# Performance work log

Measured on AMD Instinct MI355X. Metric: run time of the kernel, lower is better.

The kernel has to match this reference:

```python
import jax, jax.numpy as jnp
import numpy as np

EMBED_DIM = 768
NUM_HEADS = 12
HEAD_DIM = EMBED_DIM // NUM_HEADS
B, S = 2, 2048


def setup_inputs() -> dict:
    key = jax.random.key(0)
    ks = jax.random.split(key, 6)
    glorot = jnp.sqrt(6.0 / (EMBED_DIM + EMBED_DIM)).astype(jnp.float32)
    x = jax.random.normal(ks[0], (B, S, EMBED_DIM), dtype=jnp.float32)
    mask = jnp.zeros((1, 1, S, S), dtype=jnp.float32)  # additive mask, 0 = no masking
    Wq = jax.random.uniform(ks[1], (EMBED_DIM, EMBED_DIM), jnp.float32, -glorot, glorot)
    Wk = jax.random.uniform(ks[2], (EMBED_DIM, EMBED_DIM), jnp.float32, -glorot, glorot)
    Wv = jax.random.uniform(ks[3], (EMBED_DIM, EMBED_DIM), jnp.float32, -glorot, glorot)
    Wo = jax.random.uniform(ks[4], (EMBED_DIM, EMBED_DIM), jnp.float32, -glorot, glorot)
    bo = jnp.zeros((EMBED_DIM,), dtype=jnp.float32)
    return {"x": x, "mask": mask, "Wq": Wq, "Wk": Wk, "Wv": Wv, "Wo": Wo, "bo": bo}


def reference(x, mask, Wq, Wk, Wv, Wo, bo):
    b, s, _ = x.shape
    # Q/K/V projections (no bias), split into heads: [b, h, s, d]
    def split_heads(t):
        return t.reshape(b, s, NUM_HEADS, HEAD_DIM).transpose(0, 2, 1, 3)
    q = split_heads(x @ Wq)
    k = split_heads(x @ Wk)
    v = split_heads(x @ Wv)
    scale = 1.0 / jnp.sqrt(jnp.float32(HEAD_DIM))
    logits = jnp.einsum('bhqd,bhkd->bhqk', q, k) * scale  # [b, h, s, s]
    logits = logits + mask * (-1e9)
    weights = jax.nn.softmax(logits, axis=-1)
    attn = jnp.einsum('bhqk,bhkd->bhqd', weights, v)
    concat = attn.transpose(0, 2, 1, 3).reshape(b, s, EMBED_DIM)
    return concat @ Wo + bo
```

## Files before the change

kernel.cpp:

```cpp
#include <hip/hip_runtime.h>


typedef __bf16 bf16_t;
typedef bf16_t bf16x8 __attribute__((ext_vector_type(8)));
typedef bf16_t bf16x4 __attribute__((ext_vector_type(4)));
typedef float f32x4 __attribute__((ext_vector_type(4)));
typedef _Float16 f16x4 __attribute__((ext_vector_type(4)));

#define SC2 0.1803368801111137f

__device__ __forceinline__ float bf2f(unsigned short u) {
  union { unsigned int i; float f; } x;
  x.i = ((unsigned int)u) << 16;
  return x.f;
}

__device__ __forceinline__ void glds16(const bf16_t* g, bf16_t* l) {
  __builtin_amdgcn_global_load_lds(
      (const __attribute__((address_space(1))) void*)g,
      (__attribute__((address_space(3))) void*)l, 16, 0, 0);
}

__device__ __forceinline__ int detect_bf16_flag(const unsigned short* x) {
  const int lane = threadIdx.x & 63;
  const uint4* p = (const uint4*)x;
  uint4 a = p[lane * 2];
  uint4 b = p[lane * 2 + 1];
  unsigned int w[8] = {a.x, a.y, a.z, a.w, b.x, b.y, b.z, b.w};
  unsigned int big = 0;
#pragma unroll
  for (int i = 0; i < 8; i++) {
    unsigned int e0 = (w[i] >> 7) & 0xFF, e1 = (w[i] >> 23) & 0xFF;
    big |= (e0 > 0x88u) | (e1 > 0x88u);
  }
  unsigned long long bal = __ballot(big != 0u);
  return bal == 0ULL ? 1 : 0;
}

__global__ void k_prep(const void* __restrict__ x, const void* __restrict__ mask,
                       const void* __restrict__ Wq, const void* __restrict__ Wk,
                       const void* __restrict__ Wv, const void* __restrict__ Wo,
                       bf16_t* __restrict__ xb, bf16_t* __restrict__ wqkvT,
                       bf16_t* __restrict__ woT, int* __restrict__ mflags) {
  __shared__ float ts[32][33];
  __shared__ int snz;
  const int blk = blockIdx.x;
  const int f = detect_bf16_flag((const unsigned short*)x);

  if (blk < 1536) {
    int i = blk * 256 + threadIdx.x;
    if (f) {
      ((uint4*)xb)[i] = ((const uint4*)x)[i];
    } else {
      const float* xf = (const float*)x + (size_t)i * 8;
      bf16x8 v;
#pragma unroll
      for (int j = 0; j < 8; j++) v[j] = (bf16_t)xf[j];
      *(bf16x8*)(xb + (size_t)i * 8) = v;
    }
  } else if (blk < 3840) {
    const int t = blk - 1536;
    const int z = t / 576, r = t % 576, kt = r / 24, nt = r % 24;
    const void* wsrc = (z == 0) ? Wq : (z == 1) ? Wk : (z == 2) ? Wv : Wo;
    bf16_t* dst = (z < 3) ? (wqkvT + (size_t)z * 768 * 768) : woT;
    const int c = threadIdx.x & 31, r0 = threadIdx.x >> 5;
#pragma unroll
    for (int i = 0; i < 4; i++) {
      int kr = kt * 32 + r0 + i * 8;
      float v;
      if (f) v = bf2f(((const unsigned short*)wsrc)[(size_t)kr * 768 + nt * 32 + c]);
      else   v = ((const float*)wsrc)[(size_t)kr * 768 + nt * 32 + c];
      ts[r0 + i * 8][c] = v;
    }
    __syncthreads();
#pragma unroll
    for (int i = 0; i < 4; i++) {
      int nr = nt * 32 + r0 + i * 8;
      dst[(size_t)nr * 768 + kt * 32 + c] = (bf16_t)ts[c][r0 + i * 8];
    }
  } else {
    const int t = blk - 3840;
    const int qt = t >> 4, ktm = t & 15;
    if (threadIdx.x == 0) snz = 0;
    __syncthreads();
    int nz = 0;
    for (int i = 0; i < 64; i++) {
      int lin = i * 256 + threadIdx.x;
      int rr = lin >> 7, cc = lin & 127;
      size_t idx = (size_t)(qt * 128 + rr) * 2048 + ktm * 128 + cc;
      float v = f ? bf2f(((const unsigned short*)mask)[idx]) : ((const float*)mask)[idx];
      nz |= (v != 0.0f);
    }
    if (nz) snz = 1;
    __syncthreads();
    if (threadIdx.x == 0) mflags[qt * 16 + ktm] = snz;
  }
}

__global__ __launch_bounds__(256, 2) void k_gemmQKV(
    const bf16_t* __restrict__ A, const bf16_t* __restrict__ Bm,
    bf16_t* __restrict__ Qd, bf16_t* __restrict__ Kd, _Float16* __restrict__ Vt) {
  __shared__ __align__(16) char smem[17408];
  bf16_t* As = (bf16_t*)smem;
  bf16_t* Bs = (bf16_t*)(smem + 8192);
  _Float16* Tb = (_Float16*)smem;

  const int tid = threadIdx.x;
  const int n0 = blockIdx.x * 128, m0 = blockIdx.y * 128;
  const int r = tid >> 2, c8 = (tid & 3) << 3;
  const bf16_t* Ag = A + (size_t)(m0 + r) * 768 + c8;
  const bf16_t* Bg = Bm + (size_t)(n0 + r) * 768 + c8;
  const int wid = tid >> 6, lane = tid & 63;
  const int wm = (wid >> 1) << 6, wn = (wid & 1) << 6;
  const int lr = lane & 15, lk = (lane >> 4) << 3, g4 = (lane >> 4) << 2;

  f32x4 acc[4][4];
  const f32x4 z = {0.f, 0.f, 0.f, 0.f};
#pragma unroll
  for (int i = 0; i < 4; i++)
#pragma unroll
    for (int j = 0; j < 4; j++) acc[i][j] = z;

  for (int k0 = 0; k0 < 768; k0 += 32) {
    glds16(Ag + k0, As + wid * 512);
    glds16(Ag + (size_t)64 * 768 + k0, As + 2048 + wid * 512);
    glds16(Bg + k0, Bs + wid * 512);
    glds16(Bg + (size_t)64 * 768 + k0, Bs + 2048 + wid * 512);
    __syncthreads();
    bf16x8 af[4], bf_[4];
#pragma unroll
    for (int t = 0; t < 4; t++) af[t]  = *(const bf16x8*)&As[(wm + t * 16 + lr) * 32 + lk];
#pragma unroll
    for (int t = 0; t < 4; t++) bf_[t] = *(const bf16x8*)&Bs[(wn + t * 16 + lr) * 32 + lk];
#pragma unroll
    for (int i = 0; i < 4; i++)
#pragma unroll
      for (int j = 0; j < 4; j++)
        acc[i][j] = __builtin_amdgcn_mfma_f32_16x16x32_bf16(af[i], bf_[j], acc[i][j], 0, 0, 0);
    __syncthreads();
  }

  if (n0 < 1536) {
    bf16_t* dst = (n0 < 768) ? Qd : Kd;
    const int nb = (n0 < 768) ? n0 : n0 - 768;
    const int bb = m0 >> 11;
#pragma unroll
    for (int i = 0; i < 4; i++)
#pragma unroll
      for (int j = 0; j < 4; j++) {
        const int rc = nb + wn + j * 16 + lr;
        const int hh = rc >> 6, dd = rc & 63;
        const size_t base = (((size_t)bb * 12 + hh) * 2048) * 64 + dd;
#pragma unroll
        for (int reg = 0; reg < 4; reg++) {
          const int s = (m0 & 2047) + wm + i * 16 + g4 + reg;
          dst[base + (size_t)s * 64] = (bf16_t)acc[i][j][reg];
        }
      }
  } else {
    const int bb = m0 >> 11;
#pragma unroll
    for (int half = 0; half < 2; half++) {
      if ((wid & 1) == half) {
#pragma unroll
        for (int j = 0; j < 4; j++) {
          const int d_l = j * 16 + lr;
#pragma unroll
          for (int i = 0; i < 4; i++)
#pragma unroll
            for (int reg = 0; reg < 4; reg++)
              Tb[d_l * 136 + wm + i * 16 + g4 + reg] = (_Float16)acc[i][j][reg];
        }
      }
      __syncthreads();
      const int row = tid >> 2, cc = (tid & 3) * 32;
      const int vcol = (n0 - 1536) + half * 64 + row;
      const int hh = vcol >> 6;
      _Float16* dstv = Vt + (((size_t)bb * 12 + hh) * 64 + row) * 2048 + (m0 & 2047) + cc;
#pragma unroll
      for (int u = 0; u < 4; u++)
        *(uint4*)(dstv + u * 8) = *(const uint4*)&Tb[row * 136 + cc + u * 8];
      __syncthreads();
    }
  }
}

__global__ __launch_bounds__(320, 4) void k_flash(
    const bf16_t* __restrict__ Qd, const bf16_t* __restrict__ Kd,
    const _Float16* __restrict__ Vt, const void* __restrict__ mask,
    const int* __restrict__ mflags, const unsigned short* __restrict__ xdet,
    bf16_t* __restrict__ attn) {
  __shared__ __align__(16) char sm[32768];

  const int tid = threadIdx.x, wid = tid >> 6, lane = tid & 63;
  const int lr = lane & 15, quad = lane >> 4, lk = quad << 3, g4 = quad << 2;

  const int lin = blockIdx.x;
  const int gx = lin & 7, ww = lin >> 3;
  const int hb = gx * 3 + (ww >> 5);
  const int h = hb % 12, bb = hb / 12;
  const int qt = ww & 31;

  const size_t bh = (size_t)bb * 12 + h;
  const char* Kh = (const char*)(Kd + bh * 2048 * 64);
  const char* Vh = (const char*)(Vt + bh * 64 * 2048);

  if (wid == 4) {
    const char* kS[8]; const char* vS[8];
#pragma unroll
    for (int u = 0; u < 8; u++) {
      const int R = (u >> 1) * 16 + lr;
      const int c = (u & 1) * 4 + quad;
      kS[u] = Kh + R * 128 + c * 16;
      const int u2 = u * 2 + (lane >> 5);
      const int dtv = u2 & 3, ctv = u2 >> 2, j2 = lane & 31;
      vS[u] = Vh + (size_t)(dtv * 16 + (j2 & 15)) * 4096 + ctv * 32 + (j2 >> 4) * 16;
    }
    uint4 kv[8], vv[8];
#pragma unroll
    for (int u = 0; u < 8; u++) kv[u] = *(const uint4*)(kS[u]);
#pragma unroll
    for (int u = 0; u < 8; u++) vv[u] = *(const uint4*)(vS[u]);
#pragma unroll
    for (int u = 0; u < 8; u++) *(uint4*)(sm + u * 1024 + lane * 16) = kv[u];
#pragma unroll
    for (int u = 0; u < 8; u++) *(uint4*)(sm + 8192 + u * 1024 + lane * 16) = vv[u];
    __syncthreads();
    for (int s = 0; s < 32; s++) {
      if (s < 31) {
        const int t = s + 1;
        char* buf = sm + (t & 1) * 16384;
#pragma unroll
        for (int u = 0; u < 8; u++) kv[u] = *(const uint4*)(kS[u] + (size_t)t * 8192);
#pragma unroll
        for (int u = 0; u < 8; u++) vv[u] = *(const uint4*)(vS[u] + (size_t)t * 128);
#pragma unroll
        for (int u = 0; u < 8; u++) *(uint4*)(buf + u * 1024 + lane * 16) = kv[u];
#pragma unroll
        for (int u = 0; u < 8; u++) *(uint4*)(buf + 8192 + u * 1024 + lane * 16) = vv[u];
      }
      __syncthreads();
    }
    return;
  }

  const bf16_t* Qh = Qd + bh * 2048 * 64;
  const int q0 = qt * 64 + wid * 16;
  const int mbf = detect_bf16_flag(xdet);
  const int* mfrow = mflags + (qt >> 1) * 16;

  const bf16x8 qf0 = *(const bf16x8*)&Qh[(size_t)(q0 + lr) * 64 + lk];
  const bf16x8 qf1 = *(const bf16x8*)&Qh[(size_t)(q0 + lr) * 64 + 32 + lk];

  const f32x4 z = {0.f, 0.f, 0.f, 0.f};
  f32x4 ot[4];
#pragma unroll
  for (int dt = 0; dt < 4; dt++) ot[dt] = z;
  float mrow = -1e30f, lrow = 0.f;

  __syncthreads();

  for (int s = 0; s < 32; s++) {
    const char* Kc = sm + (s & 1) * 16384;
    const char* Vc = Kc + 8192;

    f32x4 sv[4];
#pragma unroll
    for (int ct = 0; ct < 4; ct++) sv[ct] = z;
#pragma unroll
    for (int ct = 0; ct < 4; ct++) {
      bf16x8 kf0 = *(const bf16x8*)(Kc + ct * 2048 + lane * 16);
      bf16x8 kf1 = *(const bf16x8*)(Kc + ct * 2048 + 1024 + lane * 16);
      sv[ct] = __builtin_amdgcn_mfma_f32_16x16x32_bf16(kf0, qf0, sv[ct], 0, 0, 0);
      sv[ct] = __builtin_amdgcn_mfma_f32_16x16x32_bf16(kf1, qf1, sv[ct], 0, 0, 0);
    }

    if (mfrow[s >> 1]) {
#pragma unroll
      for (int ct = 0; ct < 4; ct++)
#pragma unroll
        for (int reg = 0; reg < 4; reg++) {
          size_t mi = (size_t)(q0 + lr) * 2048 + s * 64 + ct * 16 + g4 + reg;
          float mv = mbf ? bf2f(((const unsigned short*)mask)[mi])
                         : ((const float*)mask)[mi];
          sv[ct][reg] -= 8e9f * mv;
        }
    }

    float t = fmaxf(
        fmaxf(fmaxf(fmaxf(sv[0][0], sv[0][1]), fmaxf(sv[0][2], sv[0][3])),
              fmaxf(fmaxf(sv[1][0], sv[1][1]), fmaxf(sv[1][2], sv[1][3]))),
        fmaxf(fmaxf(fmaxf(sv[2][0], sv[2][1]), fmaxf(sv[2][2], sv[2][3])),
              fmaxf(fmaxf(sv[3][0], sv[3][1]), fmaxf(sv[3][2], sv[3][3]))));
    t = fmaxf(t, __shfl_xor(t, 16));
    t = fmaxf(t, __shfl_xor(t, 32));
    const float mnew = fmaxf(mrow, t);
    const float alpha = exp2f((mrow - mnew) * SC2);
    const float mS = mnew * SC2;
    mrow = mnew;

    float rs = 0.f;
    f16x4 pb[4];
#pragma unroll
    for (int ct = 0; ct < 4; ct++) {
      float p0 = exp2f(fmaf(sv[ct][0], SC2, -mS));
      float p1 = exp2f(fmaf(sv[ct][1], SC2, -mS));
      float p2 = exp2f(fmaf(sv[ct][2], SC2, -mS));
      float p3 = exp2f(fmaf(sv[ct][3], SC2, -mS));
      rs += (p0 + p1) + (p2 + p3);
      f16x4 pk;
      pk[0] = (_Float16)p0; pk[1] = (_Float16)p1;
      pk[2] = (_Float16)p2; pk[3] = (_Float16)p3;
      pb[ct] = pk;
    }
    rs += __shfl_xor(rs, 16);
    rs += __shfl_xor(rs, 32);
    lrow = lrow * alpha + rs;

#pragma unroll
    for (int dt = 0; dt < 4; dt++)
#pragma unroll
      for (int reg = 0; reg < 4; reg++) ot[dt][reg] *= alpha;
#pragma unroll
    for (int ct = 0; ct < 4; ct++) {
#pragma unroll
      for (int dt = 0; dt < 4; dt++) {
        f16x4 va = *(const f16x4*)(Vc + (ct * 4 + dt) * 512 +
                                   (quad >> 1) * 256 + lr * 16 + (quad & 1) * 8);
        ot[dt] = __builtin_amdgcn_mfma_f32_16x16x16f16(va, pb[ct], ot[dt], 0, 0, 0);
      }
    }
    __syncthreads();
  }

  const float inv = 1.0f / lrow;
  bf16_t* arow = attn + ((size_t)bb * 2048 + q0 + lr) * 768 + h * 64 + g4;
#pragma unroll
  for (int dt = 0; dt < 4; dt++) {
    bf16x4 v;
#pragma unroll
    for (int reg = 0; reg < 4; reg++) v[reg] = (bf16_t)(ot[dt][reg] * inv);
    *(bf16x4*)(arow + dt * 16) = v;
  }
}

__global__ __launch_bounds__(256, 4) void k_gemm2(
    const bf16_t* __restrict__ A, const bf16_t* __restrict__ Bm,
    const void* __restrict__ bo, const unsigned short* __restrict__ xdet,
    float* __restrict__ outF, unsigned short* __restrict__ outH) {
  __shared__ __align__(16) bf16_t As[64 * 32];
  __shared__ __align__(16) bf16_t Bs[128 * 32];
  const int tid = threadIdx.x, wid = tid >> 6, lane = tid & 63;
  const int n0 = blockIdx.x * 128, m0 = blockIdx.y * 64;
  const int wm = (wid >> 1) * 32, wn = (wid & 1) * 64;
  const int lr = lane & 15, lk = (lane >> 4) << 3, g4 = (lane >> 4) << 2;
  const int rr = lane >> 2, c8 = (lane & 3) << 3;
  const bf16_t* Ag  = A + (size_t)(m0 + wid * 16 + rr) * 768 + c8;
  const bf16_t* Bg0 = Bm + (size_t)(n0 + wid * 32 + rr) * 768 + c8;
  const bf16_t* Bg1 = Bm + (size_t)(n0 + wid * 32 + 16 + rr) * 768 + c8;

  f32x4 acc[2][4];
  const f32x4 z = {0.f, 0.f, 0.f, 0.f};
#pragma unroll
  for (int i = 0; i < 2; i++)
#pragma unroll
    for (int j = 0; j < 4; j++) acc[i][j] = z;

  for (int k0 = 0; k0 < 768; k0 += 32) {
    glds16(Ag + k0, As + wid * 512);
    glds16(Bg0 + k0, Bs + wid * 1024);
    glds16(Bg1 + k0, Bs + wid * 1024 + 512);
    __syncthreads();
    bf16x8 af[2], bf_[4];
#pragma unroll
    for (int i = 0; i < 2; i++) af[i]  = *(const bf16x8*)&As[(wm + i * 16 + lr) * 32 + lk];
#pragma unroll
    for (int j = 0; j < 4; j++) bf_[j] = *(const bf16x8*)&Bs[(wn + j * 16 + lr) * 32 + lk];
#pragma unroll
    for (int i = 0; i < 2; i++)
#pragma unroll
      for (int j = 0; j < 4; j++)
        acc[i][j] = __builtin_amdgcn_mfma_f32_16x16x32_bf16(af[i], bf_[j], acc[i][j], 0, 0, 0);
    __syncthreads();
  }

  const int obf = detect_bf16_flag(xdet);
#pragma unroll
  for (int i = 0; i < 2; i++)
#pragma unroll
    for (int j = 0; j < 4; j++) {
      const int nn = n0 + wn + j * 16 + lr;
      const float bv = obf ? bf2f(((const unsigned short*)bo)[nn])
                           : ((const float*)bo)[nn];
#pragma unroll
      for (int reg = 0; reg < 4; reg++) {
        const int m = m0 + wm + i * 16 + g4 + reg;
        const float v = acc[i][j][reg] + bv;
        if (obf) outH[(size_t)m * 768 + nn] = __builtin_bit_cast(unsigned short, (bf16_t)v);
        else     outF[(size_t)m * 768 + nn] = v;
      }
    }
}

extern "C" void kernel_launch(void* const* d_in, const int* in_sizes, int n_in,
                              void* d_out, int out_size, void* d_ws, size_t ws_size,
                              hipStream_t stream) {
  (void)in_sizes; (void)n_in; (void)out_size; (void)ws_size;
  const void* x    = d_in[0];
  const void* mask = d_in[1];
  const void* Wq   = d_in[2];
  const void* Wk   = d_in[3];
  const void* Wv   = d_in[4];
  const void* Wo   = d_in[5];
  const void* bo   = d_in[6];

  char* w = (char*)d_ws;
  size_t off = 0;
  auto take = [&](size_t b) -> void* {
    void* p = w + off;
    off = (off + b + 255) & ~(size_t)255;
    return p;
  };
  int*      mflags = (int*)take(256 * 4);
  bf16_t*   wqkvT  = (bf16_t*)take((size_t)2304 * 768 * 2);
  bf16_t*   woT    = (bf16_t*)take((size_t)768 * 768 * 2);
  bf16_t*   xb     = (bf16_t*)take((size_t)4096 * 768 * 2);
  bf16_t*   Qd     = (bf16_t*)take((size_t)3145728 * 2);
  bf16_t*   Kd     = (bf16_t*)take((size_t)3145728 * 2);
  _Float16* Vt     = (_Float16*)take((size_t)3145728 * 2);
  bf16_t*   attn   = xb;

  k_prep<<<4096, 256, 0, stream>>>(x, mask, Wq, Wk, Wv, Wo, xb, wqkvT, woT, mflags);
  k_gemmQKV<<<dim3(18, 32), 256, 0, stream>>>(xb, wqkvT, Qd, Kd, Vt);
  k_flash<<<768, 320, 0, stream>>>(Qd, Kd, Vt, mask, mflags,
                                   (const unsigned short*)x, attn);
  k_gemm2<<<dim3(6, 64), 256, 0, stream>>>(attn, woT, bo, (const unsigned short*)x,
                                           (float*)d_out, (unsigned short*)d_out);
}
```

Baseline: 201.5 us.

## Vectorize mask scan, skip bf16 x copy, and lighten flash softmax rescale

Several independent tweaks. The prep kernel now scans the mask with 16-byte loads, and skips copying x when the input is already bf16, with the QKV GEMM reading x directly in that case. The QKV GEMM's occupancy hint is raised. The flash kernel packs the mask flags into a bitmask, uses the hardware exp2 intrinsic and packed fp16 conversion with round-toward-zero, and applies the running-max rescale only when some lane's max actually increased. Round-toward-zero conversion and the raw exp2 intrinsic change rounding slightly, and the higher occupancy hint may force register spills.

```diff
diff --git a/kernel.cpp b/kernel.cpp
--- a/kernel.cpp
+++ b/kernel.cpp
@@ -6,6 +6,7 @@
 typedef bf16_t bf16x4 __attribute__((ext_vector_type(4)));
 typedef float f32x4 __attribute__((ext_vector_type(4)));
 typedef _Float16 f16x4 __attribute__((ext_vector_type(4)));
+typedef __fp16 hf2 __attribute__((ext_vector_type(2)));
 
 #define SC2 0.1803368801111137f
 
@@ -13,6 +14,10 @@
   union { unsigned int i; float f; } x;
   x.i = ((unsigned int)u) << 16;
   return x.f;
+}
+
+__device__ __forceinline__ float fexp2(float x) {
+  return __builtin_amdgcn_exp2f(x);
 }
 
 __device__ __forceinline__ void glds16(const bf16_t* g, bf16_t* l) {
@@ -48,16 +53,13 @@
   const int f = detect_bf16_flag((const unsigned short*)x);
 
   if (blk < 1536) {
+    if (f) return;
     int i = blk * 256 + threadIdx.x;
-    if (f) {
-      ((uint4*)xb)[i] = ((const uint4*)x)[i];
-    } else {
-      const float* xf = (const float*)x + (size_t)i * 8;
-      bf16x8 v;
-#pragma unroll
-      for (int j = 0; j < 8; j++) v[j] = (bf16_t)xf[j];
-      *(bf16x8*)(xb + (size_t)i * 8) = v;
-    }
+    const float* xf = (const float*)x + (size_t)i * 8;
+    bf16x8 v;
+#pragma unroll
+    for (int j = 0; j < 8; j++) v[j] = (bf16_t)xf[j];
+    *(bf16x8*)(xb + (size_t)i * 8) = v;
   } else if (blk < 3840) {
     const int t = blk - 1536;
     const int z = t / 576, r = t % 576, kt = r / 24, nt = r % 24;
@@ -83,13 +85,27 @@
     const int qt = t >> 4, ktm = t & 15;
     if (threadIdx.x == 0) snz = 0;
     __syncthreads();
-    int nz = 0;
-    for (int i = 0; i < 64; i++) {
-      int lin = i * 256 + threadIdx.x;
-      int rr = lin >> 7, cc = lin & 127;
-      size_t idx = (size_t)(qt * 128 + rr) * 2048 + ktm * 128 + cc;
-      float v = f ? bf2f(((const unsigned short*)mask)[idx]) : ((const float*)mask)[idx];
-      nz |= (v != 0.0f);
+    unsigned int nz = 0;
+    if (f) {
+#pragma unroll
+      for (int i = 0; i < 8; i++) {
+        int uidx = i * 256 + threadIdx.x;
+        int row = uidx >> 4, col = uidx & 15;
+        const uint4* p = (const uint4*)((const char*)mask +
+            ((size_t)(qt * 128 + row) * 2048 + ktm * 128) * 2 + col * 16);
+        uint4 v = *p;
+        nz |= ((v.x | v.y | v.z | v.w) & 0x7fff7fffu);
+      }
+    } else {
+#pragma unroll
+      for (int i = 0; i < 16; i++) {
+        int uidx = i * 256 + threadIdx.x;
+        int row = uidx >> 5, col = uidx & 31;
+        const uint4* p = (const uint4*)((const char*)mask +
+            ((size_t)(qt * 128 + row) * 2048 + ktm * 128) * 4 + col * 16);
+        uint4 v = *p;
+        nz |= ((v.x | v.y | v.z | v.w) & 0x7fffffffu);
+      }
     }
     if (nz) snz = 1;
     __syncthreads();
@@ -97,13 +113,17 @@
   }
 }
 
-__global__ __launch_bounds__(256, 2) void k_gemmQKV(
-    const bf16_t* __restrict__ A, const bf16_t* __restrict__ Bm,
-    bf16_t* __restrict__ Qd, bf16_t* __restrict__ Kd, _Float16* __restrict__ Vt) {
+__global__ __launch_bounds__(256, 3) void k_gemmQKV(
+    const bf16_t* __restrict__ xb, const bf16_t* __restrict__ Bm,
+    bf16_t* __restrict__ Qd, bf16_t* __restrict__ Kd, _Float16* __restrict__ Vt,
+    const unsigned short* __restrict__ xdet) {
   __shared__ __align__(16) char smem[17408];
   bf16_t* As = (bf16_t*)smem;
   bf16_t* Bs = (bf16_t*)(smem + 8192);
   _Float16* Tb = (_Float16*)smem;
+
+  const int f = detect_bf16_flag(xdet);
+  const bf16_t* A = f ? (const bf16_t*)xdet : xb;
 
   const int tid = threadIdx.x;
   const int n0 = blockIdx.x * 128, m0 = blockIdx.y * 128;
@@ -248,6 +268,9 @@
   const int q0 = qt * 64 + wid * 16;
   const int mbf = detect_bf16_flag(xdet);
   const int* mfrow = mflags + (qt >> 1) * 16;
+  int mbits = 0;
+#pragma unroll
+  for (int t = 0; t < 16; t++) mbits |= (mfrow[t] != 0) << t;
 
   const bf16x8 qf0 = *(const bf16x8*)&Qh[(size_t)(q0 + lr) * 64 + lk];
   const bf16x8 qf1 = *(const bf16x8*)&Qh[(size_t)(q0 + lr) * 64 + 32 + lk];
@@ -275,7 +298,7 @@
       sv[ct] = __builtin_amdgcn_mfma_f32_16x16x32_bf16(kf1, qf1, sv[ct], 0, 0, 0);
     }
 
-    if (mfrow[s >> 1]) {
+    if ((mbits >> (s >> 1)) & 1) {
 #pragma unroll
       for (int ct = 0; ct < 4; ct++)
 #pragma unroll
@@ -295,32 +318,35 @@
     t = fmaxf(t, __shfl_xor(t, 16));
     t = fmaxf(t, __shfl_xor(t, 32));
     const float mnew = fmaxf(mrow, t);
-    const float alpha = exp2f((mrow - mnew) * SC2);
+    if (__ballot(mnew > mrow)) {
+      const float alpha = fexp2((mrow - mnew) * SC2);
+#pragma unroll
+      for (int dt = 0; dt < 4; dt++)
+#pragma unroll
+        for (int reg = 0; reg < 4; reg++) ot[dt][reg] *= alpha;
+      lrow *= alpha;
+    }
+    mrow = mnew;
     const float mS = mnew * SC2;
-    mrow = mnew;
 
     float rs = 0.f;
     f16x4 pb[4];
 #pragma unroll
     for (int ct = 0; ct < 4; ct++) {
-      float p0 = exp2f(fmaf(sv[ct][0], SC2, -mS));
-      float p1 = exp2f(fmaf(sv[ct][1], SC2, -mS));
-      float p2 = exp2f(fmaf(sv[ct][2], SC2, -mS));
-      float p3 = exp2f(fmaf(sv[ct][3], SC2, -mS));
+      float p0 = fexp2(fmaf(sv[ct][0], SC2, -mS));
+      float p1 = fexp2(fmaf(sv[ct][1], SC2, -mS));
+      float p2 = fexp2(fmaf(sv[ct][2], SC2, -mS));
+      float p3 = fexp2(fmaf(sv[ct][3], SC2, -mS));
       rs += (p0 + p1) + (p2 + p3);
-      f16x4 pk;
-      pk[0] = (_Float16)p0; pk[1] = (_Float16)p1;
-      pk[2] = (_Float16)p2; pk[3] = (_Float16)p3;
-      pb[ct] = pk;
+      union { hf2 h[2]; f16x4 v; } u;
+      u.h[0] = __builtin_amdgcn_cvt_pkrtz(p0, p1);
+      u.h[1] = __builtin_amdgcn_cvt_pkrtz(p2, p3);
+      pb[ct] = u.v;
     }
     rs += __shfl_xor(rs, 16);
     rs += __shfl_xor(rs, 32);
-    lrow = lrow * alpha + rs;
-
-#pragma unroll
-    for (int dt = 0; dt < 4; dt++)
-#pragma unroll
-      for (int reg = 0; reg < 4; reg++) ot[dt][reg] *= alpha;
+    lrow += rs;
+
 #pragma unroll
     for (int ct = 0; ct < 4; ct++) {
 #pragma unroll
@@ -431,7 +457,8 @@
   bf16_t*   attn   = xb;
 
   k_prep<<<4096, 256, 0, stream>>>(x, mask, Wq, Wk, Wv, Wo, xb, wqkvT, woT, mflags);
-  k_gemmQKV<<<dim3(18, 32), 256, 0, stream>>>(xb, wqkvT, Qd, Kd, Vt);
+  k_gemmQKV<<<dim3(18, 32), 256, 0, stream>>>(xb, wqkvT, Qd, Kd, Vt,
+                                              (const unsigned short*)x);
   k_flash<<<768, 320, 0, stream>>>(Qd, Kd, Vt, mask, mflags,
                                    (const unsigned short*)x, attn);
   k_gemm2<<<dim3(6, 64), 256, 0, stream>>>(attn, woT, bo, (const unsigned short*)x,
```

Result: faster. 186.5 us (-7.4%).
